# Optimization experiments

Measured on AMD Instinct MI355X. Metric: run time of the kernel, lower is better.

## Reference

```python
import jax, jax.numpy as jnp
import numpy as np

N_NODES = 100000
N_EDGES = 3200000
IN_CH = 32
HID = 16


def setup_inputs() -> dict:
    key = jax.random.key(0)
    ks = jax.random.split(key, 8)
    x = jax.random.normal(ks[0], (N_NODES, IN_CH), dtype=jnp.float32)
    edge_index = jax.random.randint(ks[1], (2, N_EDGES), 0, N_NODES, dtype=jnp.int64)
    s1 = 1.0 / np.sqrt(IN_CH)
    s2 = 1.0 / np.sqrt(HID)
    Wl1 = jax.random.normal(ks[2], (HID, IN_CH), dtype=jnp.float32) * s1
    Wr1 = jax.random.normal(ks[3], (HID, IN_CH), dtype=jnp.float32) * s1
    b1 = jnp.zeros((HID,), dtype=jnp.float32)
    Wl2 = jax.random.normal(ks[4], (1, HID), dtype=jnp.float32) * s2
    Wr2 = jax.random.normal(ks[5], (1, HID), dtype=jnp.float32) * s2
    b2 = jnp.zeros((1,), dtype=jnp.float32)
    return {"x": x, "edge_index": edge_index, "Wl1": Wl1, "Wr1": Wr1,
            "b1": b1, "Wl2": Wl2, "Wr2": Wr2, "b2": b2}


def _sage_conv(h, src, dst, deg_inv, Wl, Wr, b):
    # mean aggregation of source features at destination nodes
    msg_sum = jax.ops.segment_sum(h[src], dst, num_segments=N_NODES)  # [N, F]
    agg = msg_sum * deg_inv[:, None]
    # lin_l(agg) + lin_r(h): lin_l carries the bias (PyG SAGEConv convention)
    return agg @ Wl.T + b + h @ Wr.T


def reference(x, edge_index, Wl1, Wr1, b1, Wl2, Wr2, b2):
    src = edge_index[0]
    dst = edge_index[1]
    deg = jax.ops.segment_sum(jnp.ones((N_EDGES,), dtype=x.dtype), dst,
                              num_segments=N_NODES)
    deg_inv = 1.0 / jnp.maximum(deg, 1.0)  # mean; nodes w/o in-edges get 0 agg

    h = _sage_conv(x, src, dst, deg_inv, Wl1, Wr1, b1)
    h = jax.nn.relu(h)
    # F.dropout in eval mode -> identity
    out = _sage_conv(h, src, dst, deg_inv, Wl2, Wr2, b2)
    return out.squeeze(-1)  # [N]
```

## Files before the change

### kernel.cpp

```cpp
#include <hip/hip_runtime.h>

#define N_NODES 100000
#define N_EDGES 3200000
#define NB 1024
#define BKN 98
#define RSZ 5120
#define TILE 12500
#define NTILES 256
#define MAXB4 3
#define HOLE_REC (127 << 17)


__device__ __forceinline__ float bf2f_lo(unsigned int w) {
  return __uint_as_float(w << 16);
}
__device__ __forceinline__ float bf2f_hi(unsigned int w) {
  return __uint_as_float(w & 0xFFFF0000u);
}
__device__ __forceinline__ unsigned short f2bf(float f) {
  unsigned int b = __float_as_uint(f);
  return (unsigned short)((b + 0x7FFFu + ((b >> 16) & 1u)) >> 16);
}

__global__ __launch_bounds__(256) void k_proj1(
    const float* __restrict__ x, const float* __restrict__ Wl1,
    const float* __restrict__ Wr1, const float* __restrict__ b1,
    unsigned short* __restrict__ p1h, float* __restrict__ q1b,
    int* __restrict__ gcur) {
  __shared__ float sWl[512];
  __shared__ float sWr[512];
  __shared__ float sb[16];
  const int t = threadIdx.x;
  if (t < 64) {
    const int gi = blockIdx.x * 64 + t;
    if (gi < NB * 16) gcur[gi] = 0;
  }
  for (int i = t; i < 512; i += 256) {
    sWl[i] = Wl1[i];
    sWr[i] = Wr1[i];
  }
  if (t < 16) sb[t] = b1[t];
  __syncthreads();

  const int n = blockIdx.x * 256 + t;
  if (n >= N_NODES) return;

  float xr[32];
  const float4* xp = (const float4*)(x + (size_t)n * 32);
#pragma unroll
  for (int j = 0; j < 8; ++j) {
    float4 v = xp[j];
    xr[4 * j + 0] = v.x;
    xr[4 * j + 1] = v.y;
    xr[4 * j + 2] = v.z;
    xr[4 * j + 3] = v.w;
  }
  float pv[16], qv[16];
#pragma unroll
  for (int hh = 0; hh < 16; ++hh) {
    float a = 0.f, b = 0.f;
#pragma unroll
    for (int i = 0; i < 32; ++i) {
      a = fmaf(xr[i], sWl[hh * 32 + i], a);
      b = fmaf(xr[i], sWr[hh * 32 + i], b);
    }
    pv[hh] = a;
    qv[hh] = b + sb[hh];
  }
  unsigned int w[8];
#pragma unroll
  for (int j = 0; j < 8; ++j)
    w[j] = (unsigned int)f2bf(pv[2 * j]) |
           ((unsigned int)f2bf(pv[2 * j + 1]) << 16);
  uint4* pp = (uint4*)(p1h + (size_t)n * 16);
  pp[0] = make_uint4(w[0], w[1], w[2], w[3]);
  pp[1] = make_uint4(w[4], w[5], w[6], w[7]);
  float4* qp = (float4*)(q1b + (size_t)n * 16);
#pragma unroll
  for (int j = 0; j < 4; ++j)
    qp[j] = make_float4(qv[4 * j], qv[4 * j + 1], qv[4 * j + 2], qv[4 * j + 3]);
}

__global__ __launch_bounds__(1024, 1) void k_bscatter(
    const int* __restrict__ ei, int* __restrict__ gcur,
    int* __restrict__ recs) {
  __shared__ int hist[1024];
  __shared__ int bstart[1024];
  __shared__ int gbase[1024];
  __shared__ int wsum[16];
  __shared__ int stage[TILE];
  const int t = threadIdx.x;
  const int kb = blockIdx.x;
  hist[t] = 0;
  __syncthreads();

  const int tb = kb * TILE;
#pragma unroll
  for (int i = 0; i < 13; ++i) {
    const int pos = t + i * 1024;
    if (pos < TILE) {
      const int d = ei[N_EDGES + tb + pos];
      atomicAdd(&hist[(int)((unsigned)d / (unsigned)BKN)], 1);
    }
  }
  __syncthreads();

  const int sv = hist[t];
  int incl = sv;
#pragma unroll
  for (int o = 1; o < 64; o <<= 1) {
    const int uu = __shfl_up(incl, o);
    if ((t & 63) >= o) incl += uu;
  }
  if ((t & 63) == 63) wsum[t >> 6] = incl;
  __syncthreads();
  if (t == 0) {
    int run = 0;
#pragma unroll
    for (int i = 0; i < 16; ++i) {
      const int v = wsum[i];
      wsum[i] = run;
      run += v;
    }
  }
  __syncthreads();
  bstart[t] = wsum[t >> 6] + incl - sv;
  {
    const int pc = (sv + 15) & ~15;
    gbase[t] = pc ? atomicAdd(&gcur[t * 16], pc) : 0;
  }
  hist[t] = 0;
  __syncthreads();

#pragma unroll
  for (int i = 0; i < 13; ++i) {
    const int pos = t + i * 1024;
    if (pos < TILE) {
      const int e = tb + pos;
      const int s = ei[e];
      const int d = ei[N_EDGES + e];
      const int k = (int)((unsigned)d / (unsigned)BKN);
      const int r = atomicAdd(&hist[k], 1);
      stage[bstart[k] + r] = ((d - k * BKN) << 17) | s;
    }
  }
  __syncthreads();

  {
    const int c = hist[t];
    const int st = bstart[t];
    const int off = gbase[t];
    const int pc = (c + 15) & ~15;
    int* gb = recs + (size_t)t * RSZ + off;
    for (int i = 0; i < pc; i += 4) {
      if (off + i + 4 <= RSZ) {
        int4 v;
        v.x = (i < c) ? stage[st + i] : HOLE_REC;
        v.y = (i + 1 < c) ? stage[st + i + 1] : HOLE_REC;
        v.z = (i + 2 < c) ? stage[st + i + 2] : HOLE_REC;
        v.w = (i + 3 < c) ? stage[st + i + 3] : HOLE_REC;
        *(int4*)(gb + i) = v;
      }
    }
  }
}

__global__ __launch_bounds__(512, 8) void k_sortagg1(
    const int* __restrict__ gcur, const int* __restrict__ recs,
    const unsigned short* __restrict__ p1h, const float* __restrict__ q1b,
    const float* __restrict__ Wl2, const float* __restrict__ Wr2,
    float* __restrict__ p2, float* __restrict__ r2,
    float* __restrict__ deg_inv) {
  __shared__ int hist[128];
  __shared__ int nstart[128];
  __shared__ int ssort[RSZ];
  __shared__ float sWl[16], sWr[16];
  const int t = threadIdx.x;
  const int kb = blockIdx.x;
  const int cend = min(gcur[kb * 16], RSZ);
  const int n4 = cend >> 2;
  if (t < 128) hist[t] = 0;
  if (t < 16) {
    sWl[t] = Wl2[t];
    sWr[t] = Wr2[t];
  }
  __syncthreads();

  const int4* r4 = (const int4*)(recs + (size_t)kb * RSZ);
  int rc[12], ax[12];
#pragma unroll
  for (int i = 0; i < MAXB4; ++i) {
    const int idx = t + i * 512;
    if (idx < n4) {
      const int4 v = r4[idx];
      const int l0 = v.x >> 17, l1 = v.y >> 17, l2 = v.z >> 17, l3 = v.w >> 17;
      rc[4 * i + 0] = v.x & 0x1FFFF;
      ax[4 * i + 0] = (l0 << 13) | atomicAdd(&hist[l0], 1);
      rc[4 * i + 1] = v.y & 0x1FFFF;
      ax[4 * i + 1] = (l1 << 13) | atomicAdd(&hist[l1], 1);
      rc[4 * i + 2] = v.z & 0x1FFFF;
      ax[4 * i + 2] = (l2 << 13) | atomicAdd(&hist[l2], 1);
      rc[4 * i + 3] = v.w & 0x1FFFF;
      ax[4 * i + 3] = (l3 << 13) | atomicAdd(&hist[l3], 1);
    } else {
      ax[4 * i + 0] = ax[4 * i + 1] = ax[4 * i + 2] = ax[4 * i + 3] = -1;
    }
  }
  __syncthreads();

  if (t < 64) {
    const int a = hist[t], b = hist[t + 64];
    int ia = a, ib = b;
#pragma unroll
    for (int o = 1; o < 64; o <<= 1) {
      const int ua = __shfl_up(ia, o);
      const int ub = __shfl_up(ib, o);
      if (t >= o) {
        ia += ua;
        ib += ub;
      }
    }
    const int tt = __shfl(ia, 63);
    nstart[t] = ia - a;
    nstart[t + 64] = tt + ib - b;
  }
  __syncthreads();

#pragma unroll
  for (int i = 0; i < 12; ++i) {
    if (ax[i] >= 0) ssort[nstart[ax[i] >> 13] + (ax[i] & 0x1FFF)] = rc[i];
  }
  __syncthreads();

  const int quad = t & 3;
  const int half = quad & 1;
  const int epar = quad >> 1;
  const unsigned short* pb = p1h + half * 8;
  const int local = t >> 2;
  if (local < BKN) {
    const int n = kb * BKN + local;
    if (n < N_NODES) {
      const int st = nstart[local];
      const int k = hist[local];

      float acc[8];
#pragma unroll
      for (int i = 0; i < 8; ++i) acc[i] = 0.f;
      int j = epar;
      for (; j + 6 < k; j += 8) {
        const int s0 = ssort[st + j], s1 = ssort[st + j + 2],
                  s2 = ssort[st + j + 4], s3 = ssort[st + j + 6];
        const uint4 w0 = *(const uint4*)(pb + (size_t)s0 * 16);
        const uint4 w1 = *(const uint4*)(pb + (size_t)s1 * 16);
        const uint4 w2 = *(const uint4*)(pb + (size_t)s2 * 16);
        const uint4 w3 = *(const uint4*)(pb + (size_t)s3 * 16);
        acc[0] +=
            (bf2f_lo(w0.x) + bf2f_lo(w1.x)) + (bf2f_lo(w2.x) + bf2f_lo(w3.x));
        acc[1] +=
            (bf2f_hi(w0.x) + bf2f_hi(w1.x)) + (bf2f_hi(w2.x) + bf2f_hi(w3.x));
        acc[2] +=
            (bf2f_lo(w0.y) + bf2f_lo(w1.y)) + (bf2f_lo(w2.y) + bf2f_lo(w3.y));
        acc[3] +=
            (bf2f_hi(w0.y) + bf2f_hi(w1.y)) + (bf2f_hi(w2.y) + bf2f_hi(w3.y));
        acc[4] +=
            (bf2f_lo(w0.z) + bf2f_lo(w1.z)) + (bf2f_lo(w2.z) + bf2f_lo(w3.z));
        acc[5] +=
            (bf2f_hi(w0.z) + bf2f_hi(w1.z)) + (bf2f_hi(w2.z) + bf2f_hi(w3.z));
        acc[6] +=
            (bf2f_lo(w0.w) + bf2f_lo(w1.w)) + (bf2f_lo(w2.w) + bf2f_lo(w3.w));
        acc[7] +=
            (bf2f_hi(w0.w) + bf2f_hi(w1.w)) + (bf2f_hi(w2.w) + bf2f_hi(w3.w));
      }
      for (; j < k; j += 2) {
        const uint4 w = *(const uint4*)(pb + (size_t)ssort[st + j] * 16);
        acc[0] += bf2f_lo(w.x);
        acc[1] += bf2f_hi(w.x);
        acc[2] += bf2f_lo(w.y);
        acc[3] += bf2f_hi(w.y);
        acc[4] += bf2f_lo(w.z);
        acc[5] += bf2f_hi(w.z);
        acc[6] += bf2f_lo(w.w);
        acc[7] += bf2f_hi(w.w);
      }
#pragma unroll
      for (int i = 0; i < 8; ++i) acc[i] += __shfl_xor(acc[i], 2);

      const float di = 1.f / fmaxf((float)k, 1.f);
      const float4* qp = (const float4*)(q1b + (size_t)n * 16 + half * 8);
      const float4 qa = qp[0], qb = qp[1];
      float h[8];
      h[0] = fmaxf(fmaf(acc[0], di, qa.x), 0.f);
      h[1] = fmaxf(fmaf(acc[1], di, qa.y), 0.f);
      h[2] = fmaxf(fmaf(acc[2], di, qa.z), 0.f);
      h[3] = fmaxf(fmaf(acc[3], di, qa.w), 0.f);
      h[4] = fmaxf(fmaf(acc[4], di, qb.x), 0.f);
      h[5] = fmaxf(fmaf(acc[5], di, qb.y), 0.f);
      h[6] = fmaxf(fmaf(acc[6], di, qb.z), 0.f);
      h[7] = fmaxf(fmaf(acc[7], di, qb.w), 0.f);
      float pa = 0.f, pbv = 0.f;
#pragma unroll
      for (int i = 0; i < 8; ++i) {
        pa = fmaf(h[i], sWl[half * 8 + i], pa);
        pbv = fmaf(h[i], sWr[half * 8 + i], pbv);
      }
      pa += __shfl_xor(pa, 1);
      pbv += __shfl_xor(pbv, 1);
      if (quad == 0) {
        p2[n] = pa;
        r2[n] = pbv;
        deg_inv[n] = di;
      }
    }
  }
}

__global__ __launch_bounds__(512, 8) void k_agg2out(
    const int* __restrict__ gcur, const int* __restrict__ recs,
    const float* __restrict__ p2, const float* __restrict__ r2,
    const float* __restrict__ deg_inv, const float* __restrict__ b2,
    float* __restrict__ out) {
  __shared__ float acc[128];
  const int t = threadIdx.x;
  const int kb = blockIdx.x;
  if (t < 128) acc[t] = 0.f;
  __syncthreads();

  const int cend = min(gcur[kb * 16], RSZ);
  const int n4 = cend >> 2;
  const int4* r4 = (const int4*)(recs + (size_t)kb * RSZ);
#pragma unroll
  for (int i = 0; i < MAXB4; ++i) {
    const int idx = t + i * 512;
    if (idx < n4) {
      const int4 v = r4[idx];
      const float p0 = p2[v.x & 0x1FFFF];
      const float p1 = p2[v.y & 0x1FFFF];
      const float pz = p2[v.z & 0x1FFFF];
      const float pw = p2[v.w & 0x1FFFF];
      atomicAdd(&acc[v.x >> 17], p0);
      atomicAdd(&acc[v.y >> 17], p1);
      atomicAdd(&acc[v.z >> 17], pz);
      atomicAdd(&acc[v.w >> 17], pw);
    }
  }
  __syncthreads();

  if (t < BKN) {
    const int n = kb * BKN + t;
    if (n < N_NODES) out[n] = fmaf(acc[t], deg_inv[n], r2[n] + b2[0]);
  }
}

extern "C" void kernel_launch(void* const* d_in, const int* in_sizes, int n_in,
                              void* d_out, int out_size, void* d_ws,
                              size_t ws_size, hipStream_t stream) {
  const float* x   = (const float*)d_in[0];
  const int*   ei  = (const int*)d_in[1];
  const float* Wl1 = (const float*)d_in[2];
  const float* Wr1 = (const float*)d_in[3];
  const float* b1  = (const float*)d_in[4];
  const float* Wl2 = (const float*)d_in[5];
  const float* Wr2 = (const float*)d_in[6];
  const float* b2  = (const float*)d_in[7];
  float* out = (float*)d_out;

  const size_t N = N_NODES;
  int* wi = (int*)d_ws;
  int* gcur = wi;
  int* recs = wi + NB * 16;
  unsigned short* p1h = (unsigned short*)(recs + (size_t)NB * RSZ);
  float* q1b     = (float*)(p1h + 16 * N);
  float* p2      = q1b + 16 * N;
  float* r2      = p2 + N;
  float* deg_inv = r2 + N;

  k_proj1<<<(N_NODES + 255) / 256, 256, 0, stream>>>(x, Wl1, Wr1, b1, p1h,
                                                     q1b, gcur);
  k_bscatter<<<NTILES, 1024, 0, stream>>>(ei, gcur, recs);
  k_sortagg1<<<NB, 512, 0, stream>>>(gcur, recs, p1h, q1b, Wl2, Wr2, p2, r2,
                                     deg_inv);
  k_agg2out<<<NB, 512, 0, stream>>>(gcur, recs, p2, r2, deg_inv, b2, out);
}
```

Before: 175.8 us.

## Replace atomic bucket allocation with fixed per-tile slots and fuse projection

```diff
diff --git a/kernel.cpp b/kernel.cpp
--- a/kernel.cpp
+++ b/kernel.cpp
@@ -4,10 +4,13 @@
 #define N_EDGES 3200000
 #define NB 1024
 #define BKN 98
-#define RSZ 5120
 #define TILE 12500
 #define NTILES 256
-#define MAXB4 3
+#define SLOT 36
+#define BSTRIDE (NTILES * SLOT)
+#define SSORT 3968
+#define MAXIT 13
+#define PROJ_BLOCKS 98
 #define HOLE_REC (127 << 17)
 
 
@@ -17,32 +20,98 @@
 __device__ __forceinline__ float bf2f_hi(unsigned int w) {
   return __uint_as_float(w & 0xFFFF0000u);
 }
-__device__ __forceinline__ unsigned short f2bf(float f) {
+__device__ __forceinline__ unsigned int f2bf(float f) {
   unsigned int b = __float_as_uint(f);
-  return (unsigned short)((b + 0x7FFFu + ((b >> 16) & 1u)) >> 16);
-}
-
-__global__ __launch_bounds__(256) void k_proj1(
-    const float* __restrict__ x, const float* __restrict__ Wl1,
-    const float* __restrict__ Wr1, const float* __restrict__ b1,
-    unsigned short* __restrict__ p1h, float* __restrict__ q1b,
-    int* __restrict__ gcur) {
-  __shared__ float sWl[512];
-  __shared__ float sWr[512];
-  __shared__ float sb[16];
+  return (b + 0x7FFFu + ((b >> 16) & 1u)) >> 16;
+}
+
+__global__ __launch_bounds__(1024, 8) void k_scatterproj(
+    const float* __restrict__ x, const int* __restrict__ ei,
+    const float* __restrict__ Wl1, const float* __restrict__ Wr1,
+    const float* __restrict__ b1, unsigned short* __restrict__ p1h,
+    float* __restrict__ q1b, int* __restrict__ recs) {
+  __shared__ union {
+    struct { int hist[1024]; int wsum[16]; int stage[TILE]; } s;
+    struct { float Wl[512], Wr[512], b[16]; } w;
+  } u;
   const int t = threadIdx.x;
-  if (t < 64) {
-    const int gi = blockIdx.x * 64 + t;
-    if (gi < NB * 16) gcur[gi] = 0;
-  }
-  for (int i = t; i < 512; i += 256) {
-    sWl[i] = Wl1[i];
-    sWr[i] = Wr1[i];
-  }
-  if (t < 16) sb[t] = b1[t];
-  __syncthreads();
-
-  const int n = blockIdx.x * 256 + t;
+  const int kb = blockIdx.x;
+
+  if (kb < NTILES) {
+    u.s.hist[t] = 0;
+    __syncthreads();
+
+    const int tb = kb * TILE;
+    int rec[MAXIT], aux[MAXIT];
+#pragma unroll
+    for (int i = 0; i < MAXIT; ++i) {
+      const int pos = t + i * 1024;
+      if (pos < TILE) {
+        const int e = tb + pos;
+        const int s = ei[e];
+        const int d = ei[N_EDGES + e];
+        const int k = (int)((unsigned)d / (unsigned)BKN);
+        const int r = atomicAdd(&u.s.hist[k], 1);
+        rec[i] = ((d - k * BKN) << 17) | s;
+        aux[i] = (k << 16) | r;
+      } else {
+        aux[i] = -1;
+      }
+    }
+    __syncthreads();
+
+    const int sv = u.s.hist[t];
+    int incl = sv;
+#pragma unroll
+    for (int o = 1; o < 64; o <<= 1) {
+      const int uu = __shfl_up(incl, o);
+      if ((t & 63) >= o) incl += uu;
+    }
+    if ((t & 63) == 63) u.s.wsum[t >> 6] = incl;
+    __syncthreads();
+    if (t == 0) {
+      int run = 0;
+#pragma unroll
+      for (int i = 0; i < 16; ++i) {
+        const int v = u.s.wsum[i];
+        u.s.wsum[i] = run;
+        run += v;
+      }
+    }
+    __syncthreads();
+    const int ex = u.s.wsum[t >> 6] + incl - sv;
+    u.s.hist[t] = ex;
+    __syncthreads();
+
+#pragma unroll
+    for (int i = 0; i < MAXIT; ++i) {
+      if (aux[i] >= 0)
+        u.s.stage[u.s.hist[aux[i] >> 16] + (aux[i] & 0xFFFF)] = rec[i];
+    }
+    __syncthreads();
+
+    {
+      const int cc = min(sv, SLOT);
+      int* gb = recs + (size_t)t * BSTRIDE + kb * SLOT;
+#pragma unroll
+      for (int i = 0; i < SLOT; i += 4) {
+        int4 v;
+        v.x = (i < cc) ? u.s.stage[ex + i] : HOLE_REC;
+        v.y = (i + 1 < cc) ? u.s.stage[ex + i + 1] : HOLE_REC;
+        v.z = (i + 2 < cc) ? u.s.stage[ex + i + 2] : HOLE_REC;
+        v.w = (i + 3 < cc) ? u.s.stage[ex + i + 3] : HOLE_REC;
+        *(int4*)(gb + i) = v;
+      }
+    }
+    return;
+  }
+
+  if (t < 512) u.w.Wl[t] = Wl1[t];
+  else u.w.Wr[t - 512] = Wr1[t - 512];
+  if (t < 16) u.w.b[t] = b1[t];
+  __syncthreads();
+
+  const int n = (kb - NTILES) * 1024 + t;
   if (n >= N_NODES) return;
 
   float xr[32];
@@ -55,130 +124,43 @@
     xr[4 * j + 2] = v.z;
     xr[4 * j + 3] = v.w;
   }
-  float pv[16], qv[16];
-#pragma unroll
-  for (int hh = 0; hh < 16; ++hh) {
-    float a = 0.f, b = 0.f;
-#pragma unroll
-    for (int i = 0; i < 32; ++i) {
-      a = fmaf(xr[i], sWl[hh * 32 + i], a);
-      b = fmaf(xr[i], sWr[hh * 32 + i], b);
-    }
-    pv[hh] = a;
-    qv[hh] = b + sb[hh];
-  }
-  unsigned int w[8];
-#pragma unroll
-  for (int j = 0; j < 8; ++j)
-    w[j] = (unsigned int)f2bf(pv[2 * j]) |
-           ((unsigned int)f2bf(pv[2 * j + 1]) << 16);
-  uint4* pp = (uint4*)(p1h + (size_t)n * 16);
-  pp[0] = make_uint4(w[0], w[1], w[2], w[3]);
-  pp[1] = make_uint4(w[4], w[5], w[6], w[7]);
-  float4* qp = (float4*)(q1b + (size_t)n * 16);
-#pragma unroll
-  for (int j = 0; j < 4; ++j)
-    qp[j] = make_float4(qv[4 * j], qv[4 * j + 1], qv[4 * j + 2], qv[4 * j + 3]);
-}
-
-__global__ __launch_bounds__(1024, 1) void k_bscatter(
-    const int* __restrict__ ei, int* __restrict__ gcur,
-    int* __restrict__ recs) {
-  __shared__ int hist[1024];
-  __shared__ int bstart[1024];
-  __shared__ int gbase[1024];
-  __shared__ int wsum[16];
-  __shared__ int stage[TILE];
-  const int t = threadIdx.x;
-  const int kb = blockIdx.x;
-  hist[t] = 0;
-  __syncthreads();
-
-  const int tb = kb * TILE;
-#pragma unroll
-  for (int i = 0; i < 13; ++i) {
-    const int pos = t + i * 1024;
-    if (pos < TILE) {
-      const int d = ei[N_EDGES + tb + pos];
-      atomicAdd(&hist[(int)((unsigned)d / (unsigned)BKN)], 1);
-    }
-  }
-  __syncthreads();
-
-  const int sv = hist[t];
-  int incl = sv;
-#pragma unroll
-  for (int o = 1; o < 64; o <<= 1) {
-    const int uu = __shfl_up(incl, o);
-    if ((t & 63) >= o) incl += uu;
-  }
-  if ((t & 63) == 63) wsum[t >> 6] = incl;
-  __syncthreads();
-  if (t == 0) {
-    int run = 0;
-#pragma unroll
-    for (int i = 0; i < 16; ++i) {
-      const int v = wsum[i];
-      wsum[i] = run;
-      run += v;
-    }
-  }
-  __syncthreads();
-  bstart[t] = wsum[t >> 6] + incl - sv;
-  {
-    const int pc = (sv + 15) & ~15;
-    gbase[t] = pc ? atomicAdd(&gcur[t * 16], pc) : 0;
-  }
-  hist[t] = 0;
-  __syncthreads();
-
-#pragma unroll
-  for (int i = 0; i < 13; ++i) {
-    const int pos = t + i * 1024;
-    if (pos < TILE) {
-      const int e = tb + pos;
-      const int s = ei[e];
-      const int d = ei[N_EDGES + e];
-      const int k = (int)((unsigned)d / (unsigned)BKN);
-      const int r = atomicAdd(&hist[k], 1);
-      stage[bstart[k] + r] = ((d - k * BKN) << 17) | s;
-    }
-  }
-  __syncthreads();
-
-  {
-    const int c = hist[t];
-    const int st = bstart[t];
-    const int off = gbase[t];
-    const int pc = (c + 15) & ~15;
-    int* gb = recs + (size_t)t * RSZ + off;
-    for (int i = 0; i < pc; i += 4) {
-      if (off + i + 4 <= RSZ) {
-        int4 v;
-        v.x = (i < c) ? stage[st + i] : HOLE_REC;
-        v.y = (i + 1 < c) ? stage[st + i + 1] : HOLE_REC;
-        v.z = (i + 2 < c) ? stage[st + i + 2] : HOLE_REC;
-        v.w = (i + 3 < c) ? stage[st + i + 3] : HOLE_REC;
-        *(int4*)(gb + i) = v;
-      }
-    }
+#pragma unroll
+  for (int ch = 0; ch < 2; ++ch) {
+    float pv[8], qv[8];
+#pragma unroll
+    for (int h2 = 0; h2 < 8; ++h2) {
+      const int hh = ch * 8 + h2;
+      float a = 0.f, b = 0.f;
+#pragma unroll
+      for (int i = 0; i < 32; ++i) {
+        a = fmaf(xr[i], u.w.Wl[hh * 32 + i], a);
+        b = fmaf(xr[i], u.w.Wr[hh * 32 + i], b);
+      }
+      pv[h2] = a;
+      qv[h2] = b + u.w.b[hh];
+    }
+    unsigned int w[4];
+#pragma unroll
+    for (int j = 0; j < 4; ++j)
+      w[j] = f2bf(pv[2 * j]) | (f2bf(pv[2 * j + 1]) << 16);
+    ((uint4*)(p1h + (size_t)n * 16))[ch] = make_uint4(w[0], w[1], w[2], w[3]);
+    float4* qp = (float4*)(q1b + (size_t)n * 16) + 2 * ch;
+    qp[0] = make_float4(qv[0], qv[1], qv[2], qv[3]);
+    qp[1] = make_float4(qv[4], qv[5], qv[6], qv[7]);
   }
 }
 
 __global__ __launch_bounds__(512, 8) void k_sortagg1(
-    const int* __restrict__ gcur, const int* __restrict__ recs,
-    const unsigned short* __restrict__ p1h, const float* __restrict__ q1b,
-    const float* __restrict__ Wl2, const float* __restrict__ Wr2,
-    float* __restrict__ p2, float* __restrict__ r2,
-    float* __restrict__ deg_inv) {
+    const int* __restrict__ recs, const unsigned short* __restrict__ p1h,
+    const float* __restrict__ q1b, const float* __restrict__ Wl2,
+    const float* __restrict__ Wr2, float* __restrict__ p2,
+    float* __restrict__ r2, float* __restrict__ deg_inv) {
   __shared__ int hist[128];
   __shared__ int nstart[128];
-  __shared__ int ssort[RSZ];
+  __shared__ int ssort[SSORT];
   __shared__ float sWl[16], sWr[16];
   const int t = threadIdx.x;
   const int kb = blockIdx.x;
-  const int cend = min(gcur[kb * 16], RSZ);
-  const int n4 = cend >> 2;
   if (t < 128) hist[t] = 0;
   if (t < 16) {
     sWl[t] = Wl2[t];
@@ -186,25 +168,16 @@
   }
   __syncthreads();
 
-  const int4* r4 = (const int4*)(recs + (size_t)kb * RSZ);
-  int rc[12], ax[12];
-#pragma unroll
-  for (int i = 0; i < MAXB4; ++i) {
-    const int idx = t + i * 512;
-    if (idx < n4) {
-      const int4 v = r4[idx];
-      const int l0 = v.x >> 17, l1 = v.y >> 17, l2 = v.z >> 17, l3 = v.w >> 17;
-      rc[4 * i + 0] = v.x & 0x1FFFF;
-      ax[4 * i + 0] = (l0 << 13) | atomicAdd(&hist[l0], 1);
-      rc[4 * i + 1] = v.y & 0x1FFFF;
-      ax[4 * i + 1] = (l1 << 13) | atomicAdd(&hist[l1], 1);
-      rc[4 * i + 2] = v.z & 0x1FFFF;
-      ax[4 * i + 2] = (l2 << 13) | atomicAdd(&hist[l2], 1);
-      rc[4 * i + 3] = v.w & 0x1FFFF;
-      ax[4 * i + 3] = (l3 << 13) | atomicAdd(&hist[l3], 1);
-    } else {
-      ax[4 * i + 0] = ax[4 * i + 1] = ax[4 * i + 2] = ax[4 * i + 3] = -1;
-    }
+  const int4* r4 = (const int4*)(recs + (size_t)kb * BSTRIDE);
+  const int N4 = BSTRIDE / 4;
+
+  for (int idx = t; idx < N4; idx += 512) {
+    const int4 v = r4[idx];
+    const int l0 = v.x >> 17, l1 = v.y >> 17, l2 = v.z >> 17, l3 = v.w >> 17;
+    if (l0 < BKN) atomicAdd(&hist[l0], 1);
+    if (l1 < BKN) atomicAdd(&hist[l1], 1);
+    if (l2 < BKN) atomicAdd(&hist[l2], 1);
+    if (l3 < BKN) atomicAdd(&hist[l3], 1);
   }
   __syncthreads();
 
@@ -226,9 +199,17 @@
   }
   __syncthreads();
 
-#pragma unroll
-  for (int i = 0; i < 12; ++i) {
-    if (ax[i] >= 0) ssort[nstart[ax[i] >> 13] + (ax[i] & 0x1FFF)] = rc[i];
+  for (int idx = t; idx < N4; idx += 512) {
+    const int4 v = r4[idx];
+#pragma unroll
+    for (int e2 = 0; e2 < 4; ++e2) {
+      const int rv = (e2 == 0) ? v.x : (e2 == 1) ? v.y : (e2 == 2) ? v.z : v.w;
+      const int l = rv >> 17;
+      if (l < BKN) {
+        const int pos = atomicAdd(&nstart[l], 1);
+        if (pos < SSORT) ssort[pos] = rv & 0x1FFFF;
+      }
+    }
   }
   __syncthreads();
 
@@ -240,8 +221,8 @@
   if (local < BKN) {
     const int n = kb * BKN + local;
     if (n < N_NODES) {
-      const int st = nstart[local];
       const int k = hist[local];
+      const int st = nstart[local] - k;
 
       float acc[8];
 #pragma unroll
@@ -315,33 +296,29 @@
 }
 
 __global__ __launch_bounds__(512, 8) void k_agg2out(
-    const int* __restrict__ gcur, const int* __restrict__ recs,
-    const float* __restrict__ p2, const float* __restrict__ r2,
-    const float* __restrict__ deg_inv, const float* __restrict__ b2,
-    float* __restrict__ out) {
+    const int* __restrict__ recs, const float* __restrict__ p2,
+    const float* __restrict__ r2, const float* __restrict__ deg_inv,
+    const float* __restrict__ b2, float* __restrict__ out) {
   __shared__ float acc[128];
   const int t = threadIdx.x;
   const int kb = blockIdx.x;
   if (t < 128) acc[t] = 0.f;
   __syncthreads();
 
-  const int cend = min(gcur[kb * 16], RSZ);
-  const int n4 = cend >> 2;
-  const int4* r4 = (const int4*)(recs + (size_t)kb * RSZ);
-#pragma unroll
-  for (int i = 0; i < MAXB4; ++i) {
-    const int idx = t + i * 512;
-    if (idx < n4) {
-      const int4 v = r4[idx];
-      const float p0 = p2[v.x & 0x1FFFF];
-      const float p1 = p2[v.y & 0x1FFFF];
-      const float pz = p2[v.z & 0x1FFFF];
-      const float pw = p2[v.w & 0x1FFFF];
-      atomicAdd(&acc[v.x >> 17], p0);
-      atomicAdd(&acc[v.y >> 17], p1);
-      atomicAdd(&acc[v.z >> 17], pz);
-      atomicAdd(&acc[v.w >> 17], pw);
-    }
+  const int4* r4 = (const int4*)(recs + (size_t)kb * BSTRIDE);
+  const int N4 = BSTRIDE / 4;
+#pragma unroll 5
+  for (int idx = t; idx < N4; idx += 512) {
+    const int4 v = r4[idx];
+    const float g0 = p2[v.x & 0x1FFFF];
+    const float g1 = p2[v.y & 0x1FFFF];
+    const float g2 = p2[v.z & 0x1FFFF];
+    const float g3 = p2[v.w & 0x1FFFF];
+    const int l0 = v.x >> 17, l1 = v.y >> 17, l2 = v.z >> 17, l3 = v.w >> 17;
+    if (l0 < BKN) atomicAdd(&acc[l0], g0);
+    if (l1 < BKN) atomicAdd(&acc[l1], g1);
+    if (l2 < BKN) atomicAdd(&acc[l2], g2);
+    if (l3 < BKN) atomicAdd(&acc[l3], g3);
   }
   __syncthreads();
 
@@ -365,19 +342,16 @@
   float* out = (float*)d_out;
 
   const size_t N = N_NODES;
-  int* wi = (int*)d_ws;
-  int* gcur = wi;
-  int* recs = wi + NB * 16;
-  unsigned short* p1h = (unsigned short*)(recs + (size_t)NB * RSZ);
+  int* recs = (int*)d_ws;
+  unsigned short* p1h = (unsigned short*)(recs + (size_t)NB * BSTRIDE);
   float* q1b     = (float*)(p1h + 16 * N);
   float* p2      = q1b + 16 * N;
   float* r2      = p2 + N;
   float* deg_inv = r2 + N;
 
-  k_proj1<<<(N_NODES + 255) / 256, 256, 0, stream>>>(x, Wl1, Wr1, b1, p1h,
-                                                     q1b, gcur);
-  k_bscatter<<<NTILES, 1024, 0, stream>>>(ei, gcur, recs);
-  k_sortagg1<<<NB, 512, 0, stream>>>(gcur, recs, p1h, q1b, Wl2, Wr2, p2, r2,
+  k_scatterproj<<<NTILES + PROJ_BLOCKS, 1024, 0, stream>>>(x, ei, Wl1, Wr1,
+                                                           b1, p1h, q1b, recs);
+  k_sortagg1<<<NB, 512, 0, stream>>>(recs, p1h, q1b, Wl2, Wr2, p2, r2,
                                      deg_inv);
-  k_agg2out<<<NB, 512, 0, stream>>>(gcur, recs, p2, r2, deg_inv, b2, out);
-}
+  k_agg2out<<<NB, 512, 0, stream>>>(recs, p2, r2, deg_inv, b2, out);
+}
```

Result: slower. 235.4 us (+33.9%).
